# Performance work log

Hardware: AMD Instinct MI355X
Metric: run time of the kernel (lower is better)

The kernel has to match this reference:

```python
import jax, jax.numpy as jnp
import numpy as np

L, B, D, H = 2048, 2, 1024, 16
DK = D // H
SCALE = DK ** -0.5


def setup_inputs() -> dict:
    key = jax.random.key(0)
    ks = jax.random.split(key, 11)
    w_std = D ** -0.5
    return {
        "query": jax.random.normal(ks[0], (L, B, D), dtype=jnp.float32),
        "key": jax.random.normal(ks[1], (L, B, D), dtype=jnp.float32),
        "value": jax.random.normal(ks[2], (L, B, D), dtype=jnp.float32),
        "WQ_w": jax.random.normal(ks[3], (D, D), dtype=jnp.float32) * w_std,
        "WQ_b": jnp.zeros((D,), dtype=jnp.float32),
        "WK_w": jax.random.normal(ks[4], (D, D), dtype=jnp.float32) * w_std,
        "WK_b": jnp.zeros((D,), dtype=jnp.float32),
        "WV_w": jax.random.normal(ks[5], (D, D), dtype=jnp.float32) * w_std,
        "WV_b": jnp.zeros((D,), dtype=jnp.float32),
        "WO_w": jax.random.normal(ks[6], (D, D), dtype=jnp.float32) * w_std,
        "WO_b": jnp.zeros((D,), dtype=jnp.float32),
    }


def reference(query, key, value, WQ_w, WQ_b, WK_w, WK_b, WV_w, WV_b, WO_w, WO_b):
    tgt_len, batch, _ = query.shape
    src_len = key.shape[0]
    # linear projections (torch Linear: x @ W^T + b)
    q = (query @ WQ_w.T + WQ_b) * SCALE            # [L, B, D]
    k = key @ WK_w.T + WK_b                        # [S, B, D]
    v = value @ WV_w.T + WV_b                      # [S, B, D]
    # split heads: [len, B, D] -> [B*H, len, DK]
    q = q.reshape(tgt_len, batch * H, DK).transpose(1, 0, 2)
    k = k.reshape(src_len, batch * H, DK).transpose(1, 0, 2)
    v = v.reshape(src_len, batch * H, DK).transpose(1, 0, 2)
    # attention scores and softmax (full [B*H, L, S] matrix, as in the original)
    scores = jnp.einsum('nld,nsd->nls', q, k)      # [B*H, L, S]
    probs = jax.nn.softmax(scores, axis=-1)
    out = jnp.einsum('nls,nsd->nld', probs, v)     # [B*H, L, DK]
    # merge heads: [B*H, L, DK] -> [L, B, D]
    out = out.transpose(1, 0, 2).reshape(tgt_len, batch, D)
    return out @ WO_w.T + WO_b
```

## Files before the change

kernel.cpp:

```cpp
#include <hip/hip_runtime.h>
#include <hip/hip_fp16.h>

#define LL 2048
#define BB 2
#define DD 1024
#define HH 16
#define DKK 64

typedef _Float16 h8 __attribute__((ext_vector_type(8)));
typedef _Float16 h4 __attribute__((ext_vector_type(4)));
typedef float f4 __attribute__((ext_vector_type(4)));
typedef float f16v __attribute__((ext_vector_type(16)));

#define BAR() do {                                              \
    asm volatile("s_waitcnt lgkmcnt(0)" ::: "memory");          \
    __builtin_amdgcn_s_barrier();                               \
    asm volatile("" ::: "memory");                              \
} while (0)

__device__ __forceinline__ void gload_lds16(const void* g, void* l) {
    __builtin_amdgcn_global_load_lds(
        (const __attribute__((address_space(1))) void*)g,
        (__attribute__((address_space(3))) void*)l, 16, 0, 0);
}

__device__ __forceinline__ unsigned pack2h(float a, float b) {
    union { __fp16 v __attribute__((ext_vector_type(2))); unsigned u; } x;
    x.v = __builtin_amdgcn_cvt_pkrtz(a, b);
    return x.u;
}

__global__ __launch_bounds__(256) void cvt_all(
    const float* __restrict__ x0, const float* __restrict__ x1,
    const float* __restrict__ x2, const float* __restrict__ w0,
    const float* __restrict__ w1, const float* __restrict__ w2,
    const float* __restrict__ w3,
    _Float16* __restrict__ y0, _Float16* __restrict__ y1,
    _Float16* __restrict__ y2, _Float16* __restrict__ z0,
    _Float16* __restrict__ z1, _Float16* __restrict__ z2,
    _Float16* __restrict__ z3)
{
    const int sel = blockIdx.y;
    if (sel >= 3 && blockIdx.x >= 512) return;
    const float* src = (sel == 0) ? x0 : (sel == 1) ? x1 : (sel == 2) ? x2
                     : (sel == 3) ? w0 : (sel == 4) ? w1 : (sel == 5) ? w2 : w3;
    _Float16* dst = (sel == 0) ? y0 : (sel == 1) ? y1 : (sel == 2) ? y2
                  : (sel == 3) ? z0 : (sel == 4) ? z1 : (sel == 5) ? z2 : z3;
    const int i = (blockIdx.x * 256 + threadIdx.x) * 8;
    f4 a = *(const f4*)(src + i);
    f4 b = *(const f4*)(src + i + 4);
    h8 o = {(_Float16)a.x, (_Float16)a.y, (_Float16)a.z, (_Float16)a.w,
            (_Float16)b.x, (_Float16)b.y, (_Float16)b.z, (_Float16)b.w};
    *(h8*)(dst + i) = o;
}

__global__ __launch_bounds__(256) void qkv_proj(
    const _Float16* __restrict__ xq, const _Float16* __restrict__ xk,
    const _Float16* __restrict__ xv,
    const _Float16* __restrict__ wq, const float* __restrict__ bq,
    const _Float16* __restrict__ wk, const float* __restrict__ bk,
    const _Float16* __restrict__ wv, const float* __restrict__ bv,
    _Float16* __restrict__ qh, _Float16* __restrict__ kh,
    _Float16* __restrict__ vth)
{
    const int mode = blockIdx.z;
    const _Float16* X    = (mode == 0) ? xq : (mode == 1) ? xk : xv;
    const _Float16* W    = (mode == 0) ? wq : (mode == 1) ? wk : wv;
    const float*    bias = (mode == 0) ? bq : (mode == 1) ? bk : bv;

    __shared__ alignas(16) _Float16 a_sm[128 * 32];
    __shared__ alignas(16) _Float16 b_sm[128 * 32];

    const int tid  = threadIdx.x;
    const int lane = tid & 63;
    const int wave = tid >> 6;
    const int wm = (wave & 1) * 64;
    const int wn = (wave >> 1) * 64;
    const int m0 = blockIdx.x * 128;
    const int n0 = blockIdx.y * 128;

    const int srow = tid >> 2;
    const int scol = (tid & 3) * 8;
    const int lds_base = wave * 512;

    f4 acc[4][4];
    #pragma unroll
    for (int i = 0; i < 4; i++)
        #pragma unroll
        for (int j = 0; j < 4; j++)
            #pragma unroll
            for (int r = 0; r < 4; r++) acc[i][j][r] = 0.f;

    const int fr = lane & 15;
    const int fk = (lane >> 4) * 8;

    for (int k0 = 0; k0 < DD; k0 += 32) {
        gload_lds16(X + (size_t)(m0 + srow) * DD + k0 + scol,       &a_sm[lds_base]);
        gload_lds16(X + (size_t)(m0 + 64 + srow) * DD + k0 + scol,  &a_sm[2048 + lds_base]);
        gload_lds16(W + (size_t)(n0 + srow) * DD + k0 + scol,       &b_sm[lds_base]);
        gload_lds16(W + (size_t)(n0 + 64 + srow) * DD + k0 + scol,  &b_sm[2048 + lds_base]);
        __syncthreads();
        h8 af[4], bfr[4];
        #pragma unroll
        for (int i = 0; i < 4; i++) af[i]  = *(const h8*)&a_sm[(wm + i * 16 + fr) * 32 + fk];
        #pragma unroll
        for (int j = 0; j < 4; j++) bfr[j] = *(const h8*)&b_sm[(wn + j * 16 + fr) * 32 + fk];
        #pragma unroll
        for (int i = 0; i < 4; i++)
            #pragma unroll
            for (int j = 0; j < 4; j++)
                acc[i][j] = __builtin_amdgcn_mfma_f32_16x16x32_f16(af[i], bfr[j], acc[i][j], 0, 0, 0);
        __syncthreads();
    }

    const int colc = lane & 15;
    const int rowb = (lane >> 4) * 4;
    #pragma unroll
    for (int i = 0; i < 4; i++) {
        #pragma unroll
        for (int j = 0; j < 4; j++) {
            const int nn = n0 + wn + j * 16 + colc;
            const float bval = bias[nn];
            #pragma unroll
            for (int reg = 0; reg < 4; reg++) {
                const int mm = m0 + wm + i * 16 + rowb + reg;
                float v = acc[i][j][reg] + bval;
                const int b = mm & 1, l = mm >> 1;
                const int h = nn >> 6, dk = nn & 63;
                const int head = b * HH + h;
                if (mode == 0) {
                    v *= 0.1803368801111243f;
                    qh[((size_t)head * LL + l) * DKK + dk] = (_Float16)v;
                } else if (mode == 1) {
                    kh[((size_t)head * LL + l) * DKK + dk] = (_Float16)v;
                } else {
                    vth[((size_t)head * DKK + dk) * LL + l] = (_Float16)v;
                }
            }
        }
    }
}

__global__ __launch_bounds__(256, 4) void attn(
    const _Float16* __restrict__ qh, const _Float16* __restrict__ kh,
    const _Float16* __restrict__ vth, _Float16* __restrict__ oh)
{
    const int head = blockIdx.y;
    const int q0   = blockIdx.x * 64;
    const int tid = threadIdx.x, lane = tid & 63, wave = tid >> 6;
    const int qs = wave & 1;
    const int sw = wave >> 1;
    const int qw = q0 + qs * 32;

    __shared__ alignas(16) char smem[36864 + 512];
    _Float16* ksm  = (_Float16*)smem;
    _Float16* vtsm = (_Float16*)(smem + 18432);

    const int rq = lane & 31;
    const int hi = lane >> 5;
    const int kb = hi * 8;
    const int tid8 = tid * 8;

    const _Float16* khead  = kh  + (size_t)head * LL * DKK;
    const _Float16* vthead = vth + (size_t)head * DKK * LL;

    const _Float16* qbase = qh + ((size_t)head * LL + qw + rq) * DKK;
    h8 qa[4];
    #pragma unroll
    for (int kf = 0; kf < 4; kf++) qa[kf] = *(const h8*)(qbase + kf * 16 + kb);

    f16v o0, o1;
    #pragma unroll
    for (int r = 0; r < 16; r++) { o0[r] = 0.f; o1[r] = 0.f; }
    float lsum = 0.f;

    #pragma unroll
    for (int b2 = 0; b2 < 2; b2++) {
        #pragma unroll
        for (int i = 0; i < 2; i++) {
            const int flat = i * 2048 + tid8;
            const int row = flat >> 6, col = flat & 63;
            *(h8*)&ksm[b2 * 4608 + row * 72 + col] =
                *(const h8*)(khead + (size_t)(b2 * 64 + row) * DKK + col);
            *(h8*)&vtsm[b2 * 4608 + row * 72 + col] =
                *(const h8*)(vthead + (size_t)row * LL + b2 * 64 + col);
        }
    }
    BAR();

    const int koff = sw * 4608;

    for (int it = 0; it < 16; ++it) {
        const int s1 = it * 128 + 128;
        const bool more = (s1 < LL);

        h8 kpre[2][2], vpre[2][2];
        if (more) {
            #pragma unroll
            for (int b2 = 0; b2 < 2; b2++) {
                #pragma unroll
                for (int i = 0; i < 2; i++) {
                    const int flat = i * 2048 + tid8;
                    const int row = flat >> 6, col = flat & 63;
                    kpre[b2][i] = *(const h8*)(khead + (size_t)(s1 + b2 * 64 + row) * DKK + col);
                    vpre[b2][i] = *(const h8*)(vthead + (size_t)row * LL + s1 + b2 * 64 + col);
                }
            }
        }

        #pragma unroll
        for (int st = 0; st < 2; st++) {
            f16v sc;
            #pragma unroll
            for (int r = 0; r < 16; r++) sc[r] = 0.f;
            #pragma unroll
            for (int kf = 0; kf < 4; kf++) {
                h8 kf8 = *(const h8*)&ksm[koff + (st * 32 + rq) * 72 + kf * 16 + kb];
                sc = __builtin_amdgcn_mfma_f32_32x32x16_f16(kf8, qa[kf], sc, 0, 0, 0);
            }

            float p[16];
            #pragma unroll
            for (int r = 0; r < 16; r++) {
                p[r] = __builtin_amdgcn_exp2f(sc[r]);
                lsum += p[r];
            }
            unsigned own[4][2], part[4][2];
            #pragma unroll
            for (int g = 0; g < 4; g++) {
                own[g][0] = pack2h(p[4 * g],     p[4 * g + 1]);
                own[g][1] = pack2h(p[4 * g + 2], p[4 * g + 3]);
                part[g][0] = __shfl_xor(own[g][0], 32, 64);
                part[g][1] = __shfl_xor(own[g][1], 32, 64);
            }
            #pragma unroll
            for (int f = 0; f < 2; f++) {
                union { unsigned u[4]; h8 h; } pa;
                pa.u[0] = hi ? part[2 * f + 1][0] : own[2 * f][0];
                pa.u[1] = hi ? part[2 * f + 1][1] : own[2 * f][1];
                pa.u[2] = hi ? own[2 * f + 1][0]  : part[2 * f][0];
                pa.u[3] = hi ? own[2 * f + 1][1]  : part[2 * f][1];
                const int vcol = st * 32 + f * 16 + kb;
                h8 b0 = *(const h8*)&vtsm[koff + rq * 72 + vcol];
                h8 b1 = *(const h8*)&vtsm[koff + (32 + rq) * 72 + vcol];
                o0 = __builtin_amdgcn_mfma_f32_32x32x16_f16(pa.h, b0, o0, 0, 0, 0);
                o1 = __builtin_amdgcn_mfma_f32_32x32x16_f16(pa.h, b1, o1, 0, 0, 0);
            }
        }

        BAR();
        if (more) {
            #pragma unroll
            for (int b2 = 0; b2 < 2; b2++) {
                #pragma unroll
                for (int i = 0; i < 2; i++) {
                    const int flat = i * 2048 + tid8;
                    const int row = flat >> 6, col = flat & 63;
                    *(h8*)&ksm[b2 * 4608 + row * 72 + col]  = kpre[b2][i];
                    *(h8*)&vtsm[b2 * 4608 + row * 72 + col] = vpre[b2][i];
                }
            }
            BAR();
        }
    }

    lsum += __shfl_xor(lsum, 32, 64);

    float* comb = (float*)smem;
    float* lsp  = (float*)(smem + 16384);
    float* invp = (float*)(smem + 16640);

    if (wave >= 2) {
        float* c = comb + qs * 2048;
        #pragma unroll
        for (int r = 0; r < 16; r++) {
            const int row = (r & 3) + 8 * (r >> 2) + 4 * hi;
            c[row * 64 + rq]      = o0[r];
            c[row * 64 + 32 + rq] = o1[r];
        }
        if (hi == 0) lsp[qs * 32 + rq] = lsum;
    }
    BAR();
    if (wave < 2) {
        lsum += lsp[qs * 32 + rq];
        invp[qs * 32 + rq] = 1.0f / lsum;
        asm volatile("s_waitcnt lgkmcnt(0)" ::: "memory");
        const int b = head >> 4, h = head & 15;
        const float* c = comb + qs * 2048;
        #pragma unroll
        for (int r = 0; r < 16; r++) {
            const int row = (r & 3) + 8 * (r >> 2) + 4 * hi;
            const float inv = invp[qs * 32 + row];
            const int ql = qw + row;
            const size_t base = (size_t)(ql * BB + b) * DD + h * DKK;
            oh[base + rq]      = (_Float16)((o0[r] + c[row * 64 + rq]) * inv);
            oh[base + 32 + rq] = (_Float16)((o1[r] + c[row * 64 + 32 + rq]) * inv);
        }
    }
}

__global__ __launch_bounds__(256) void out_proj(
    const _Float16* __restrict__ oh, const _Float16* __restrict__ wo,
    const float* __restrict__ bo, float* __restrict__ out)
{
    __shared__ alignas(16) _Float16 a_sm[64 * 32];
    __shared__ alignas(16) _Float16 b_sm[128 * 32];
    const int tid = threadIdx.x, lane = tid & 63, wave = tid >> 6;
    const int wm = (wave & 1) * 32, wn = (wave >> 1) * 64;
    const int m0 = blockIdx.x * 64, n0 = blockIdx.y * 128;

    const int srow = tid >> 2;
    const int scol = (tid & 3) * 8;
    const int lds_base = wave * 512;

    f4 acc[2][4];
    #pragma unroll
    for (int i = 0; i < 2; i++)
        #pragma unroll
        for (int j = 0; j < 4; j++)
            #pragma unroll
            for (int r = 0; r < 4; r++) acc[i][j][r] = 0.f;

    const int fr = lane & 15;
    const int fk = (lane >> 4) * 8;

    for (int k0 = 0; k0 < DD; k0 += 32) {
        gload_lds16(oh + (size_t)(m0 + srow) * DD + k0 + scol,      &a_sm[lds_base]);
        gload_lds16(wo + (size_t)(n0 + srow) * DD + k0 + scol,      &b_sm[lds_base]);
        gload_lds16(wo + (size_t)(n0 + 64 + srow) * DD + k0 + scol, &b_sm[2048 + lds_base]);
        __syncthreads();
        h8 af[2], bfr[4];
        #pragma unroll
        for (int i = 0; i < 2; i++) af[i]  = *(const h8*)&a_sm[(wm + i * 16 + fr) * 32 + fk];
        #pragma unroll
        for (int j = 0; j < 4; j++) bfr[j] = *(const h8*)&b_sm[(wn + j * 16 + fr) * 32 + fk];
        #pragma unroll
        for (int i = 0; i < 2; i++)
            #pragma unroll
            for (int j = 0; j < 4; j++)
                acc[i][j] = __builtin_amdgcn_mfma_f32_16x16x32_f16(af[i], bfr[j], acc[i][j], 0, 0, 0);
        __syncthreads();
    }

    const int colc = lane & 15;
    const int rowb = (lane >> 4) * 4;
    #pragma unroll
    for (int i = 0; i < 2; i++) {
        #pragma unroll
        for (int j = 0; j < 4; j++) {
            const int nn = n0 + wn + j * 16 + colc;
            const float bval = bo[nn];
            #pragma unroll
            for (int reg = 0; reg < 4; reg++) {
                const int mm = m0 + wm + i * 16 + rowb + reg;
                out[(size_t)mm * DD + nn] = acc[i][j][reg] + bval;
            }
        }
    }
}

extern "C" void kernel_launch(void* const* d_in, const int* in_sizes, int n_in,
                              void* d_out, int out_size, void* d_ws, size_t ws_size,
                              hipStream_t stream) {
    const float* qin = (const float*)d_in[0];
    const float* kin = (const float*)d_in[1];
    const float* vin = (const float*)d_in[2];
    const float* wq  = (const float*)d_in[3];
    const float* bq  = (const float*)d_in[4];
    const float* wk  = (const float*)d_in[5];
    const float* bk  = (const float*)d_in[6];
    const float* wv  = (const float*)d_in[7];
    const float* bv  = (const float*)d_in[8];
    const float* wo  = (const float*)d_in[9];
    const float* bo  = (const float*)d_in[10];

    const size_t seg = (size_t)32 * LL * DKK;
    _Float16* qh  = (_Float16*)d_ws;
    _Float16* kh  = qh + seg;
    _Float16* vth = kh + seg;
    _Float16* oh  = vth + seg;
    _Float16* wqh = oh + seg;
    _Float16* wkh = wqh + (size_t)DD * DD;
    _Float16* wvh = wkh + (size_t)DD * DD;
    _Float16* woh = wvh + (size_t)DD * DD;
    _Float16* xqh = woh + (size_t)DD * DD;
    _Float16* xkh = xqh + seg;
    _Float16* xvh = xkh + seg;

    hipLaunchKernelGGL(cvt_all, dim3(2048, 7), dim3(256), 0, stream,
                       qin, kin, vin, wq, wk, wv, wo,
                       xqh, xkh, xvh, wqh, wkh, wvh, woh);
    hipLaunchKernelGGL(qkv_proj, dim3(32, 8, 3), dim3(256), 0, stream,
                       xqh, xkh, xvh, wqh, bq, wkh, bk, wvh, bv, qh, kh, vth);
    hipLaunchKernelGGL(attn, dim3(32, 32), dim3(256), 0, stream, qh, kh, vth, oh);
    hipLaunchKernelGGL(out_proj, dim3(64, 8), dim3(256), 0, stream, oh, woh,
                       bo, (float*)d_out);
}
```

Baseline: 231.5 us.

## Fuse input fp16 conversion into QKV projection and pre-swizzle Q/K for register loads

```diff
diff --git a/kernel.cpp b/kernel.cpp
--- a/kernel.cpp
+++ b/kernel.cpp
@@ -8,9 +8,9 @@
 #define DKK 64
 
 typedef _Float16 h8 __attribute__((ext_vector_type(8)));
-typedef _Float16 h4 __attribute__((ext_vector_type(4)));
 typedef float f4 __attribute__((ext_vector_type(4)));
 typedef float f16v __attribute__((ext_vector_type(16)));
+typedef unsigned u2 __attribute__((ext_vector_type(2)));
 
 #define BAR() do {                                              \
     asm volatile("s_waitcnt lgkmcnt(0)" ::: "memory");          \
@@ -30,22 +30,20 @@
     return x.u;
 }
 
-__global__ __launch_bounds__(256) void cvt_all(
-    const float* __restrict__ x0, const float* __restrict__ x1,
-    const float* __restrict__ x2, const float* __restrict__ w0,
-    const float* __restrict__ w1, const float* __restrict__ w2,
-    const float* __restrict__ w3,
-    _Float16* __restrict__ y0, _Float16* __restrict__ y1,
-    _Float16* __restrict__ y2, _Float16* __restrict__ z0,
-    _Float16* __restrict__ z1, _Float16* __restrict__ z2,
-    _Float16* __restrict__ z3)
+__device__ __forceinline__ size_t swz(int head, int l, int dk) {
+    return ((((size_t)(head * 64 + (l >> 5)) * 4 + (dk >> 4)) * 2 +
+             ((dk >> 3) & 1)) * 32 + (l & 31)) * 8 + (dk & 7);
+}
+
+__global__ __launch_bounds__(256) void cvt_w(
+    const float* __restrict__ w0, const float* __restrict__ w1,
+    const float* __restrict__ w2, const float* __restrict__ w3,
+    _Float16* __restrict__ z0, _Float16* __restrict__ z1,
+    _Float16* __restrict__ z2, _Float16* __restrict__ z3)
 {
     const int sel = blockIdx.y;
-    if (sel >= 3 && blockIdx.x >= 512) return;
-    const float* src = (sel == 0) ? x0 : (sel == 1) ? x1 : (sel == 2) ? x2
-                     : (sel == 3) ? w0 : (sel == 4) ? w1 : (sel == 5) ? w2 : w3;
-    _Float16* dst = (sel == 0) ? y0 : (sel == 1) ? y1 : (sel == 2) ? y2
-                  : (sel == 3) ? z0 : (sel == 4) ? z1 : (sel == 5) ? z2 : z3;
+    const float* src = (sel == 0) ? w0 : (sel == 1) ? w1 : (sel == 2) ? w2 : w3;
+    _Float16* dst = (sel == 0) ? z0 : (sel == 1) ? z1 : (sel == 2) ? z2 : z3;
     const int i = (blockIdx.x * 256 + threadIdx.x) * 8;
     f4 a = *(const f4*)(src + i);
     f4 b = *(const f4*)(src + i + 4);
@@ -55,20 +53,20 @@
 }
 
 __global__ __launch_bounds__(256) void qkv_proj(
-    const _Float16* __restrict__ xq, const _Float16* __restrict__ xk,
-    const _Float16* __restrict__ xv,
+    const float* __restrict__ xq, const float* __restrict__ xk,
+    const float* __restrict__ xv,
     const _Float16* __restrict__ wq, const float* __restrict__ bq,
     const _Float16* __restrict__ wk, const float* __restrict__ bk,
     const _Float16* __restrict__ wv, const float* __restrict__ bv,
-    _Float16* __restrict__ qh, _Float16* __restrict__ kh,
+    _Float16* __restrict__ qhf, _Float16* __restrict__ khf,
     _Float16* __restrict__ vth)
 {
     const int mode = blockIdx.z;
-    const _Float16* X    = (mode == 0) ? xq : (mode == 1) ? xk : xv;
+    const float*    X    = (mode == 0) ? xq : (mode == 1) ? xk : xv;
     const _Float16* W    = (mode == 0) ? wq : (mode == 1) ? wk : wv;
     const float*    bias = (mode == 0) ? bq : (mode == 1) ? bk : bv;
 
-    __shared__ alignas(16) _Float16 a_sm[128 * 32];
+    __shared__ alignas(16) _Float16 a_sm[128 * 40];
     __shared__ alignas(16) _Float16 b_sm[128 * 32];
 
     const int tid  = threadIdx.x;
@@ -79,9 +77,11 @@
     const int m0 = blockIdx.x * 128;
     const int n0 = blockIdx.y * 128;
 
-    const int srow = tid >> 2;
-    const int scol = (tid & 3) * 8;
-    const int lds_base = wave * 512;
+    const int srowA = tid >> 3;
+    const int scolA = (tid & 7) * 4;
+    const int srowB = tid >> 2;
+    const int scolB = (tid & 3) * 8;
+    const int ldsB  = wave * 512;
 
     f4 acc[4][4];
     #pragma unroll
@@ -95,14 +95,18 @@
     const int fk = (lane >> 4) * 8;
 
     for (int k0 = 0; k0 < DD; k0 += 32) {
-        gload_lds16(X + (size_t)(m0 + srow) * DD + k0 + scol,       &a_sm[lds_base]);
-        gload_lds16(X + (size_t)(m0 + 64 + srow) * DD + k0 + scol,  &a_sm[2048 + lds_base]);
-        gload_lds16(W + (size_t)(n0 + srow) * DD + k0 + scol,       &b_sm[lds_base]);
-        gload_lds16(W + (size_t)(n0 + 64 + srow) * DD + k0 + scol,  &b_sm[2048 + lds_base]);
+        gload_lds16(W + (size_t)(n0 + srowB) * DD + k0 + scolB,      &b_sm[ldsB]);
+        gload_lds16(W + (size_t)(n0 + 64 + srowB) * DD + k0 + scolB, &b_sm[2048 + ldsB]);
+        #pragma unroll
+        for (int r = 0; r < 4; r++) {
+            f4 va = *(const f4*)(X + (size_t)(m0 + srowA + 32 * r) * DD + k0 + scolA);
+            u2 pk = {pack2h(va.x, va.y), pack2h(va.z, va.w)};
+            *(u2*)&a_sm[(srowA + 32 * r) * 40 + scolA] = pk;
+        }
         __syncthreads();
         h8 af[4], bfr[4];
         #pragma unroll
-        for (int i = 0; i < 4; i++) af[i]  = *(const h8*)&a_sm[(wm + i * 16 + fr) * 32 + fk];
+        for (int i = 0; i < 4; i++) af[i]  = *(const h8*)&a_sm[(wm + i * 16 + fr) * 40 + fk];
         #pragma unroll
         for (int j = 0; j < 4; j++) bfr[j] = *(const h8*)&b_sm[(wn + j * 16 + fr) * 32 + fk];
         #pragma unroll
@@ -130,9 +134,9 @@
                 const int head = b * HH + h;
                 if (mode == 0) {
                     v *= 0.1803368801111243f;
-                    qh[((size_t)head * LL + l) * DKK + dk] = (_Float16)v;
+                    qhf[swz(head, l, dk)] = (_Float16)v;
                 } else if (mode == 1) {
-                    kh[((size_t)head * LL + l) * DKK + dk] = (_Float16)v;
+                    khf[swz(head, l, dk)] = (_Float16)v;
                 } else {
                     vth[((size_t)head * DKK + dk) * LL + l] = (_Float16)v;
                 }
@@ -141,8 +145,8 @@
     }
 }
 
-__global__ __launch_bounds__(256, 4) void attn(
-    const _Float16* __restrict__ qh, const _Float16* __restrict__ kh,
+__global__ __launch_bounds__(256, 3) void attn(
+    const _Float16* __restrict__ qhf, const _Float16* __restrict__ khf,
     const _Float16* __restrict__ vth, _Float16* __restrict__ oh)
 {
     const int head = blockIdx.y;
@@ -152,22 +156,22 @@
     const int sw = wave >> 1;
     const int qw = q0 + qs * 32;
 
-    __shared__ alignas(16) char smem[36864 + 512];
-    _Float16* ksm  = (_Float16*)smem;
-    _Float16* vtsm = (_Float16*)(smem + 18432);
+    __shared__ alignas(16) char smem[37376];
+    _Float16* vtsm = (_Float16*)smem;
 
     const int rq = lane & 31;
     const int hi = lane >> 5;
-    const int kb = hi * 8;
     const int tid8 = tid * 8;
 
-    const _Float16* khead  = kh  + (size_t)head * LL * DKK;
     const _Float16* vthead = vth + (size_t)head * DKK * LL;
 
-    const _Float16* qbase = qh + ((size_t)head * LL + qw + rq) * DKK;
+    const _Float16* qbase = qhf + (size_t)(head * 64 + (qw >> 5)) * 2048;
     h8 qa[4];
     #pragma unroll
-    for (int kf = 0; kf < 4; kf++) qa[kf] = *(const h8*)(qbase + kf * 16 + kb);
+    for (int kf = 0; kf < 4; kf++)
+        qa[kf] = *(const h8*)(qbase + kf * 512 + hi * 256 + rq * 8);
+
+    const _Float16* kbase0 = khf + (size_t)(head * 64) * 2048;
 
     f16v o0, o1;
     #pragma unroll
@@ -175,38 +179,43 @@
     float lsum = 0.f;
 
     #pragma unroll
-    for (int b2 = 0; b2 < 2; b2++) {
+    for (int b2 = 0; b2 < 2; b2++)
         #pragma unroll
         for (int i = 0; i < 2; i++) {
             const int flat = i * 2048 + tid8;
             const int row = flat >> 6, col = flat & 63;
-            *(h8*)&ksm[b2 * 4608 + row * 72 + col] =
-                *(const h8*)(khead + (size_t)(b2 * 64 + row) * DKK + col);
             *(h8*)&vtsm[b2 * 4608 + row * 72 + col] =
                 *(const h8*)(vthead + (size_t)row * LL + b2 * 64 + col);
         }
-    }
     BAR();
 
-    const int koff = sw * 4608;
-
     for (int it = 0; it < 16; ++it) {
+        const int p = it & 1;
         const int s1 = it * 128 + 128;
         const bool more = (s1 < LL);
 
-        h8 kpre[2][2], vpre[2][2];
+        const _Float16* kb = kbase0 + (size_t)(it * 4 + sw * 2) * 2048;
+        h8 kc[2][4];
+        #pragma unroll
+        for (int st = 0; st < 2; st++)
+            #pragma unroll
+            for (int kf = 0; kf < 4; kf++)
+                kc[st][kf] = *(const h8*)(kb + st * 2048 + kf * 512 + hi * 256 + rq * 8);
+
+        h8 vpre[4];
         if (more) {
             #pragma unroll
-            for (int b2 = 0; b2 < 2; b2++) {
+            for (int b2 = 0; b2 < 2; b2++)
                 #pragma unroll
                 for (int i = 0; i < 2; i++) {
                     const int flat = i * 2048 + tid8;
                     const int row = flat >> 6, col = flat & 63;
-                    kpre[b2][i] = *(const h8*)(khead + (size_t)(s1 + b2 * 64 + row) * DKK + col);
-                    vpre[b2][i] = *(const h8*)(vthead + (size_t)row * LL + s1 + b2 * 64 + col);
+                    vpre[b2 * 2 + i] =
+                        *(const h8*)(vthead + (size_t)row * LL + s1 + b2 * 64 + col);
                 }
-            }
-        }
+        }
+
+        const _Float16* vb = vtsm + p * 9216 + sw * 4608;
 
         #pragma unroll
         for (int st = 0; st < 2; st++) {
@@ -214,61 +223,70 @@
             #pragma unroll
             for (int r = 0; r < 16; r++) sc[r] = 0.f;
             #pragma unroll
-            for (int kf = 0; kf < 4; kf++) {
-                h8 kf8 = *(const h8*)&ksm[koff + (st * 32 + rq) * 72 + kf * 16 + kb];
-                sc = __builtin_amdgcn_mfma_f32_32x32x16_f16(kf8, qa[kf], sc, 0, 0, 0);
+            for (int kf = 0; kf < 4; kf++)
+                sc = __builtin_amdgcn_mfma_f32_32x32x16_f16(kc[st][kf], qa[kf], sc, 0, 0, 0);
+
+            float pr[16];
+            #pragma unroll
+            for (int r = 0; r < 16; r++) {
+                pr[r] = __builtin_amdgcn_exp2f(sc[r]);
+                lsum += pr[r];
             }
-
-            float p[16];
-            #pragma unroll
-            for (int r = 0; r < 16; r++) {
-                p[r] = __builtin_amdgcn_exp2f(sc[r]);
-                lsum += p[r];
+            unsigned own[4][2];
+            #pragma unroll
+            for (int g = 0; g < 4; g++) {
+                own[g][0] = pack2h(pr[4 * g],     pr[4 * g + 1]);
+                own[g][1] = pack2h(pr[4 * g + 2], pr[4 * g + 3]);
             }
-            unsigned own[4][2], part[4][2];
-            #pragma unroll
-            for (int g = 0; g < 4; g++) {
-                own[g][0] = pack2h(p[4 * g],     p[4 * g + 1]);
-                own[g][1] = pack2h(p[4 * g + 2], p[4 * g + 3]);
-                part[g][0] = __shfl_xor(own[g][0], 32, 64);
-                part[g][1] = __shfl_xor(own[g][1], 32, 64);
-            }
-            #pragma unroll
-            for (int f = 0; f < 2; f++) {
-                union { unsigned u[4]; h8 h; } pa;
-                pa.u[0] = hi ? part[2 * f + 1][0] : own[2 * f][0];
-                pa.u[1] = hi ? part[2 * f + 1][1] : own[2 * f][1];
-                pa.u[2] = hi ? own[2 * f + 1][0]  : part[2 * f][0];
-                pa.u[3] = hi ? own[2 * f + 1][1]  : part[2 * f][1];
-                const int vcol = st * 32 + f * 16 + kb;
-                h8 b0 = *(const h8*)&vtsm[koff + rq * 72 + vcol];
-                h8 b1 = *(const h8*)&vtsm[koff + (32 + rq) * 72 + vcol];
-                o0 = __builtin_amdgcn_mfma_f32_32x32x16_f16(pa.h, b0, o0, 0, 0, 0);
-                o1 = __builtin_amdgcn_mfma_f32_32x32x16_f16(pa.h, b1, o1, 0, 0, 0);
-            }
-        }
-
-        BAR();
+            unsigned X0 = hi ? own[0][0] : own[1][0];
+            unsigned X1 = hi ? own[0][1] : own[1][1];
+            unsigned Y0 = hi ? own[2][0] : own[3][0];
+            unsigned Y1 = hi ? own[2][1] : own[3][1];
+            const unsigned rX0 = __shfl_xor(X0, 32, 64);
+            const unsigned rX1 = __shfl_xor(X1, 32, 64);
+            const unsigned rY0 = __shfl_xor(Y0, 32, 64);
+            const unsigned rY1 = __shfl_xor(Y1, 32, 64);
+
+            union { unsigned u[4]; h8 h; } pa0, pa1;
+            pa0.u[0] = hi ? rX0 : own[0][0];
+            pa0.u[1] = hi ? rX1 : own[0][1];
+            pa0.u[2] = hi ? own[1][0] : rX0;
+            pa0.u[3] = hi ? own[1][1] : rX1;
+            pa1.u[0] = hi ? rY0 : own[2][0];
+            pa1.u[1] = hi ? rY1 : own[2][1];
+            pa1.u[2] = hi ? own[3][0] : rY0;
+            pa1.u[3] = hi ? own[3][1] : rY1;
+
+            const int vc0 = st * 32 + hi * 8;
+            h8 b00 = *(const h8*)&vb[rq * 72 + vc0];
+            h8 b10 = *(const h8*)&vb[(32 + rq) * 72 + vc0];
+            o0 = __builtin_amdgcn_mfma_f32_32x32x16_f16(pa0.h, b00, o0, 0, 0, 0);
+            o1 = __builtin_amdgcn_mfma_f32_32x32x16_f16(pa0.h, b10, o1, 0, 0, 0);
+            h8 b01 = *(const h8*)&vb[rq * 72 + vc0 + 16];
+            h8 b11 = *(const h8*)&vb[(32 + rq) * 72 + vc0 + 16];
+            o0 = __builtin_amdgcn_mfma_f32_32x32x16_f16(pa1.h, b01, o0, 0, 0, 0);
+            o1 = __builtin_amdgcn_mfma_f32_32x32x16_f16(pa1.h, b11, o1, 0, 0, 0);
+        }
+
         if (more) {
-            #pragma unroll
-            for (int b2 = 0; b2 < 2; b2++) {
+            _Float16* wbuf = vtsm + (p ^ 1) * 9216;
+            #pragma unroll
+            for (int b2 = 0; b2 < 2; b2++)
                 #pragma unroll
                 for (int i = 0; i < 2; i++) {
                     const int flat = i * 2048 + tid8;
                     const int row = flat >> 6, col = flat & 63;
-                    *(h8*)&ksm[b2 * 4608 + row * 72 + col]  = kpre[b2][i];
-                    *(h8*)&vtsm[b2 * 4608 + row * 72 + col] = vpre[b2][i];
+                    *(h8*)&wbuf[b2 * 4608 + row * 72 + col] = vpre[b2 * 2 + i];
                 }
-            }
-            BAR();
-        }
+        }
+        BAR();
     }
 
     lsum += __shfl_xor(lsum, 32, 64);
 
     float* comb = (float*)smem;
-    float* lsp  = (float*)(smem + 16384);
-    float* invp = (float*)(smem + 16640);
+    float* lsp  = (float*)(smem + 36864);
+    float* invp = (float*)(smem + 37120);
 
     if (wave >= 2) {
         float* c = comb + qs * 2048;
@@ -375,24 +393,20 @@
     const float* bo  = (const float*)d_in[10];
 
     const size_t seg = (size_t)32 * LL * DKK;
-    _Float16* qh  = (_Float16*)d_ws;
-    _Float16* kh  = qh + seg;
-    _Float16* vth = kh + seg;
+    _Float16* qhf = (_Float16*)d_ws;
+    _Float16* khf = qhf + seg;
+    _Float16* vth = khf + seg;
     _Float16* oh  = vth + seg;
     _Float16* wqh = oh + seg;
     _Float16* wkh = wqh + (size_t)DD * DD;
     _Float16* wvh = wkh + (size_t)DD * DD;
     _Float16* woh = wvh + (size_t)DD * DD;
-    _Float16* xqh = woh + (size_t)DD * DD;
-    _Float16* xkh = xqh + seg;
-    _Float16* xvh = xkh + seg;
-
-    hipLaunchKernelGGL(cvt_all, dim3(2048, 7), dim3(256), 0, stream,
-                       qin, kin, vin, wq, wk, wv, wo,
-                       xqh, xkh, xvh, wqh, wkh, wvh, woh);
+
+    hipLaunchKernelGGL(cvt_w, dim3(512, 4), dim3(256), 0, stream,
+                       wq, wk, wv, wo, wqh, wkh, wvh, woh);
     hipLaunchKernelGGL(qkv_proj, dim3(32, 8, 3), dim3(256), 0, stream,
-                       xqh, xkh, xvh, wqh, bq, wkh, bk, wvh, bv, qh, kh, vth);
-    hipLaunchKernelGGL(attn, dim3(32, 32), dim3(256), 0, stream, qh, kh, vth, oh);
+                       qin, kin, vin, wqh, bq, wkh, bk, wvh, bv, qhf, khf, vth);
+    hipLaunchKernelGGL(attn, dim3(32, 32), dim3(256), 0, stream, qhf, khf, vth, oh);
     hipLaunchKernelGGL(out_proj, dim3(64, 8), dim3(256), 0, stream, oh, woh,
                        bo, (float*)d_out);
 }
```

New measurement: 267.8 us. +15.7%, slower.
